# Optimization experiments

Hardware: AMD Instinct MI355X
Metric: run time of the kernel (lower is better)

The kernel has to match this reference:

```python
import jax, jax.numpy as jnp
import numpy as np

D_MODEL = 256
D_INNER = 512   # expand_factor * d_model
D_STATE = 64
DT_RANK = 4     # ceil(d_model / 64)
D_CONV = 4
B = 8
L = 144


def setup_inputs() -> dict:
    key = jax.random.key(0)
    ks = jax.random.split(key, 8)
    s = lambda k, shp, sc=0.02: jax.random.normal(k, shp, jnp.float32) * sc
    x = jax.random.normal(ks[0], (B, L, D_MODEL), jnp.float32)
    lastin = jnp.zeros((B, D_INNER, D_STATE), jnp.float32)  # accepted but unused by the scan
    W_in = s(ks[1], (2 * D_INNER, D_MODEL))              # in_proj (no bias)
    conv_w = s(ks[2], (D_INNER, 1, D_CONV), 0.1)          # depthwise conv kernel [O, I/groups, K]
    conv_b = jnp.zeros((D_INNER,), jnp.float32)
    W_x = s(ks[3], (DT_RANK + 2 * D_STATE, D_INNER))      # x_proj (no bias)
    W_dt = s(ks[4], (D_INNER, DT_RANK), 0.1)
    b_dt = jnp.full((D_INNER,), -4.0, jnp.float32)        # softplus -> small dt, like mamba init
    A_log = jnp.log(jnp.tile(jnp.arange(1, D_STATE + 1, dtype=jnp.float32), (D_INNER, 1)))
    Dp = jnp.ones((D_INNER,), jnp.float32)
    W_out = s(ks[5], (D_MODEL, D_INNER))                  # out_proj (no bias)
    return dict(x=x, lastin=lastin, W_in=W_in, conv_w=conv_w, conv_b=conv_b,
                W_x=W_x, W_dt=W_dt, b_dt=b_dt, A_log=A_log, Dp=Dp, W_out=W_out)


def _forward(x, lastin, W_in, conv_w, conv_b, W_x, W_dt, b_dt, A_log, Dp, W_out):
    # in_proj and split
    xz = jnp.einsum('bld,ed->ble', x, W_in)               # [B, L, 2*d_inner]
    ix, z = jnp.split(xz, 2, axis=-1)

    # depthwise causal-ish conv1d: torch padding=2 then slice [:L] == padding (2, 1)
    ix = jnp.swapaxes(ix, 1, 2)                            # [B, d_inner, L]
    ix = jax.lax.conv_general_dilated(
        ix, conv_w, window_strides=(1,), padding=[(2, 1)],
        feature_group_count=D_INNER, dimension_numbers=('NCH', 'OIH', 'NCH'))
    ix = ix + conv_b[None, :, None]
    ix = jnp.swapaxes(ix, 1, 2)                            # [B, L, d_inner]
    ix = jax.nn.silu(ix)

    # ssm parameterization
    A = -jnp.exp(A_log)                                    # [d_inner, d_state]
    dBC = jnp.einsum('bld,ed->ble', ix, W_x)               # [B, L, dt_rank + 2*d_state]
    dt_r = dBC[..., :DT_RANK]
    Bm = dBC[..., DT_RANK:DT_RANK + D_STATE]               # [B, L, d_state]
    Cm = dBC[..., DT_RANK + D_STATE:]                      # [B, L, d_state]
    delta = jax.nn.softplus(jnp.einsum('blr,dr->bld', dt_r, W_dt) + b_dt)  # [B, L, d_inner]

    # discretization
    deltaA = jnp.exp(delta[..., None] * A)                 # [B, L, d_inner, d_state]
    BX = (delta * ix)[..., None] * Bm[:, :, None, :]       # [B, L, d_inner, d_state]

    # sequential selective scan: h_t = deltaA_t * h_{t-1} + BX_t
    def step(h, inp):
        dA_t, bx_t = inp
        h = dA_t * h + bx_t
        return h, h

    h0 = jnp.zeros((x.shape[0], D_INNER, D_STATE), x.dtype)
    _, hs = jax.lax.scan(step, h0, (jnp.moveaxis(deltaA, 1, 0), jnp.moveaxis(BX, 1, 0)))
    # hs: [L, B, d_inner, d_state]

    y = jnp.einsum('lbdn,lbn->bld', hs, jnp.moveaxis(Cm, 1, 0))  # [B, L, d_inner]
    y = y + Dp * ix

    out = jnp.einsum('bld,ed->ble', y * jax.nn.silu(z), W_out)   # [B, L, d_model]
    return out


def reference(x, lastin, W_in, conv_w, conv_b, W_x, W_dt, b_dt, A_log, Dp, W_out):
    return _forward(x, lastin, W_in, conv_w, conv_b, W_x, W_dt, b_dt, A_log, Dp, W_out)
```

## Files before the change

kernel.cpp:

```cpp
#include <hip/hip_runtime.h>
#include <hip/hip_bf16.h>

#define B_SZ 8
#define L_SEQ 144
#define NTOK 1152
#define D_MODEL 256
#define D_INNER 512
#define D_STATE 64
#define DT_RANK 4

typedef __attribute__((ext_vector_type(8))) short bf16x8;
typedef __attribute__((ext_vector_type(4))) float f32x4;
typedef __attribute__((ext_vector_type(4))) short short4v;

__device__ __forceinline__ unsigned short bf16_rn(float f) {
    unsigned u = __float_as_uint(f);
    u += 0x7FFF + ((u >> 16) & 1);
    return (unsigned short)(u >> 16);
}
__device__ __forceinline__ float bf16_f(unsigned short h) {
    return __uint_as_float(((unsigned)h) << 16);
}
__device__ __forceinline__ unsigned packsplit(float f) {
    const unsigned short h = bf16_rn(f);
    const unsigned short l = bf16_rn(f - bf16_f(h));
    return (unsigned)h | ((unsigned)l << 16);
}

#define LP 40

template<bool APACK, bool GN>
__global__ __launch_bounds__(256) void gemm_mfma(const void* __restrict__ Aptr,
                                                 const float* __restrict__ Bptr,
                                                 float* __restrict__ C,
                                                 const int N, const int K,
                                                 const int lda, const int ldb,
                                                 const int ldc) {
    __shared__ short Ah[64 * LP], Al[64 * LP], Bh[64 * LP], Bl[64 * LP];
    const float* Af = (const float*)Aptr;
    const unsigned* Au = (const unsigned*)Aptr;
    const int tid = threadIdx.x;
    const int m0 = blockIdx.y * 64;
    const int n0 = blockIdx.x * 64;
    const int w = tid >> 6, l = tid & 63;
    const int lm = l & 15, lq = l >> 4;
    const int m0w = (w >> 1) * 32, n0w = (w & 1) * 32;
    f32x4 acc[2][2] = {};

    for (int k0 = 0; k0 < K; k0 += 32) {
        unsigned short ha[2][4], la[2][4], hb[2][4], lb[2][4];
#pragma unroll
        for (int p = 0; p < 2; ++p) {
            const int i = tid + 256 * p;
            const int r = i >> 3, c = (i & 7) * 4;
            if (APACK) {
                const uint4 v = *(const uint4*)(Au + (size_t)(m0 + r) * lda + k0 + c);
                ha[p][0] = v.x & 0xFFFF; la[p][0] = v.x >> 16;
                ha[p][1] = v.y & 0xFFFF; la[p][1] = v.y >> 16;
                ha[p][2] = v.z & 0xFFFF; la[p][2] = v.z >> 16;
                ha[p][3] = v.w & 0xFFFF; la[p][3] = v.w >> 16;
            } else {
                const float4 v = *(const float4*)(Af + (size_t)(m0 + r) * lda + k0 + c);
                ha[p][0] = bf16_rn(v.x); la[p][0] = bf16_rn(v.x - bf16_f(ha[p][0]));
                ha[p][1] = bf16_rn(v.y); la[p][1] = bf16_rn(v.y - bf16_f(ha[p][1]));
                ha[p][2] = bf16_rn(v.z); la[p][2] = bf16_rn(v.z - bf16_f(ha[p][2]));
                ha[p][3] = bf16_rn(v.w); la[p][3] = bf16_rn(v.w - bf16_f(ha[p][3]));
            }
            float4 bv = make_float4(0.f, 0.f, 0.f, 0.f);
            if (!GN || (n0 + r) < N)
                bv = *(const float4*)(Bptr + (size_t)(n0 + r) * ldb + k0 + c);
            hb[p][0] = bf16_rn(bv.x); lb[p][0] = bf16_rn(bv.x - bf16_f(hb[p][0]));
            hb[p][1] = bf16_rn(bv.y); lb[p][1] = bf16_rn(bv.y - bf16_f(hb[p][1]));
            hb[p][2] = bf16_rn(bv.z); lb[p][2] = bf16_rn(bv.z - bf16_f(hb[p][2]));
            hb[p][3] = bf16_rn(bv.w); lb[p][3] = bf16_rn(bv.w - bf16_f(hb[p][3]));
        }
        __syncthreads();
#pragma unroll
        for (int p = 0; p < 2; ++p) {
            const int i = tid + 256 * p;
            const int r = i >> 3, c = (i & 7) * 4;
            const int o = r * LP + c;
            short4v v;
            v = (short4v){(short)ha[p][0], (short)ha[p][1], (short)ha[p][2], (short)ha[p][3]};
            *(short4v*)&Ah[o] = v;
            v = (short4v){(short)la[p][0], (short)la[p][1], (short)la[p][2], (short)la[p][3]};
            *(short4v*)&Al[o] = v;
            v = (short4v){(short)hb[p][0], (short)hb[p][1], (short)hb[p][2], (short)hb[p][3]};
            *(short4v*)&Bh[o] = v;
            v = (short4v){(short)lb[p][0], (short)lb[p][1], (short)lb[p][2], (short)lb[p][3]};
            *(short4v*)&Bl[o] = v;
        }
        __syncthreads();
        bf16x8 fah[2], fal[2], fbh[2], fbl[2];
#pragma unroll
        for (int t = 0; t < 2; ++t) {
            const int ao = (m0w + t * 16 + lm) * LP + lq * 8;
            fah[t] = *(const bf16x8*)&Ah[ao];
            fal[t] = *(const bf16x8*)&Al[ao];
            const int bo = (n0w + t * 16 + lm) * LP + lq * 8;
            fbh[t] = *(const bf16x8*)&Bh[bo];
            fbl[t] = *(const bf16x8*)&Bl[bo];
        }
#pragma unroll
        for (int mt = 0; mt < 2; ++mt)
#pragma unroll
            for (int nt = 0; nt < 2; ++nt) {
                acc[mt][nt] = __builtin_amdgcn_mfma_f32_16x16x32_bf16(
                    fal[mt], fbh[nt], acc[mt][nt], 0, 0, 0);
                acc[mt][nt] = __builtin_amdgcn_mfma_f32_16x16x32_bf16(
                    fah[mt], fbl[nt], acc[mt][nt], 0, 0, 0);
                acc[mt][nt] = __builtin_amdgcn_mfma_f32_16x16x32_bf16(
                    fah[mt], fbh[nt], acc[mt][nt], 0, 0, 0);
            }
    }
#pragma unroll
    for (int mt = 0; mt < 2; ++mt) {
        const int gm = m0 + m0w + mt * 16 + lq * 4;
#pragma unroll
        for (int nt = 0; nt < 2; ++nt) {
            const int gn = n0 + n0w + nt * 16 + lm;
            if (!GN || gn < N) {
#pragma unroll
                for (int r = 0; r < 4; ++r)
                    C[(size_t)(gm + r) * ldc + gn] = acc[mt][nt][r];
            }
        }
    }
}

__global__ __launch_bounds__(256) void transpack_k(const float* __restrict__ in,
                                                   unsigned* __restrict__ out) {
    __shared__ unsigned T[64][65];
    const int t0 = blockIdx.x * 64, d0 = blockIdx.y * 64;
    const int a = threadIdx.x & 15, g = threadIdx.x >> 4;
#pragma unroll
    for (int p = 0; p < 4; ++p) {
        const int d = g + 16 * p;
        const float4 v = *(const float4*)(in + (size_t)(d0 + d) * NTOK + t0 + a * 4);
        T[d][a * 4 + 0] = packsplit(v.x);
        T[d][a * 4 + 1] = packsplit(v.y);
        T[d][a * 4 + 2] = packsplit(v.z);
        T[d][a * 4 + 3] = packsplit(v.w);
    }
    __syncthreads();
#pragma unroll
    for (int p = 0; p < 4; ++p) {
        const int tt = g + 16 * p;
        uint4 o;
        o.x = T[a * 4 + 0][tt];
        o.y = T[a * 4 + 1][tt];
        o.z = T[a * 4 + 2][tt];
        o.w = T[a * 4 + 3][tt];
        *(uint4*)(out + (size_t)(t0 + tt) * D_INNER + d0 + a * 4) = o;
    }
}

__global__ __launch_bounds__(128) void conv_k(const float* __restrict__ xzT,
                                              const float* __restrict__ cw,
                                              const float* __restrict__ cb,
                                              float* __restrict__ ixT) {
    const int tok = blockIdx.x * 128 + threadIdx.x;
    const int d = blockIdx.y;
    const int b = tok / L_SEQ;
    const int t = tok - b * L_SEQ;
    const float* row = xzT + (size_t)d * NTOK + tok;
    const float4 w = *(const float4*)(cw + d * 4);
    float s = cb[d];
    if (t >= 2) s = fmaf(w.x, row[-2], s);
    if (t >= 1) s = fmaf(w.y, row[-1], s);
    s = fmaf(w.z, row[0], s);
    if (t < L_SEQ - 1) s = fmaf(w.w, row[1], s);
    ixT[(size_t)d * NTOK + tok] = s * __builtin_amdgcn_rcpf(1.f + __expf(-s));
}

template<int CNT>
__device__ __forceinline__ void scan_chunk(const float* __restrict__ dBC,
                                           const float* __restrict__ xzT,
                                           const float* __restrict__ ixT,
                                           float* __restrict__ gT,
                                           float4* __restrict__ aux_w,
                                           float (*__restrict__ Pw)[65],
                                           const int d, const int base, const int t0,
                                           const float An2, const float4 wdt,
                                           const float bdt, const float dpv,
                                           const int lane, float& h) {
    if (lane < CNT) {
        const int tok = base + t0 + lane;
        const float4 dt4 = *(const float4*)(dBC + (size_t)tok * 132);
        float s = fmaf(dt4.x, wdt.x, bdt);
        s = fmaf(dt4.y, wdt.y, s);
        s = fmaf(dt4.z, wdt.z, s);
        s = fmaf(dt4.w, wdt.w, s);
        const float delta = fmaxf(s, 0.f) + __logf(1.f + __expf(-fabsf(s)));
        const float ixv = ixT[(size_t)d * NTOK + tok];
        const float zv  = xzT[(size_t)(D_INNER + d) * NTOK + tok];
        const float sz  = zv * __builtin_amdgcn_rcpf(1.f + __expf(-zv));
        aux_w[lane] = make_float4(delta, delta * ixv, dpv * ixv, sz);
    }
#pragma unroll 8
    for (int i = 0; i < CNT; ++i) {
        const size_t rb = (size_t)(base + t0 + i) * 132;
        const float Bv = dBC[rb + DT_RANK + lane];
        const float Cv = dBC[rb + DT_RANK + D_STATE + lane];
        const float4 a4 = aux_w[i];
        const float dA = __builtin_amdgcn_exp2f(a4.x * An2);
        h = fmaf(dA, h, a4.y * Bv);
        Pw[i][lane] = h * Cv;
    }
    const int tl = lane & 31, hf = lane >> 5;
    float s2 = 0.f;
    if (tl < CNT) {
#pragma unroll
        for (int j = 0; j < 32; ++j) s2 += Pw[tl][hf * 32 + j];
    }
    s2 += __shfl_xor(s2, 32, 64);
    if (hf == 0 && tl < CNT) {
        const float4 a4 = aux_w[tl];
        gT[(size_t)d * NTOK + base + t0 + tl] = (s2 + a4.z) * a4.w;
    }
}

__global__ __launch_bounds__(256) void scan_k(const float* __restrict__ dBC,
                                              const float* __restrict__ xzT,
                                              const float* __restrict__ ixT,
                                              const float* __restrict__ W_dt,
                                              const float* __restrict__ b_dt,
                                              const float* __restrict__ A_log,
                                              const float* __restrict__ Dp,
                                              float* __restrict__ gT) {
    __shared__ float4 aux_s[4][32];
    __shared__ float P[4][32][65];
    const int w = threadIdx.x >> 6, lane = threadIdx.x & 63;
    const int b = blockIdx.x >> 7, dg = blockIdx.x & 127;
    const int d = (dg << 2) | w;
    const int base = b * L_SEQ;
    const float An2 = -__expf(A_log[(d << 6) + lane]) * 1.44269504088896f;
    const float4 wdt = *(const float4*)(W_dt + (d << 2));
    const float bdt = b_dt[d], dpv = Dp[d];
    float h = 0.f;
    scan_chunk<32>(dBC, xzT, ixT, gT, aux_s[w], P[w], d, base, 0,  An2, wdt, bdt, dpv, lane, h);
    scan_chunk<32>(dBC, xzT, ixT, gT, aux_s[w], P[w], d, base, 32, An2, wdt, bdt, dpv, lane, h);
    scan_chunk<32>(dBC, xzT, ixT, gT, aux_s[w], P[w], d, base, 64, An2, wdt, bdt, dpv, lane, h);
    scan_chunk<32>(dBC, xzT, ixT, gT, aux_s[w], P[w], d, base, 96, An2, wdt, bdt, dpv, lane, h);
    scan_chunk<16>(dBC, xzT, ixT, gT, aux_s[w], P[w], d, base, 128, An2, wdt, bdt, dpv, lane, h);
}

extern "C" void kernel_launch(void* const* d_in, const int* in_sizes, int n_in,
                              void* d_out, int out_size, void* d_ws, size_t ws_size,
                              hipStream_t stream) {
    const float* x      = (const float*)d_in[0];
    const float* W_in   = (const float*)d_in[2];
    const float* conv_w = (const float*)d_in[3];
    const float* conv_b = (const float*)d_in[4];
    const float* W_x    = (const float*)d_in[5];
    const float* W_dt   = (const float*)d_in[6];
    const float* b_dt   = (const float*)d_in[7];
    const float* A_log  = (const float*)d_in[8];
    const float* Dp     = (const float*)d_in[9];
    const float* W_out  = (const float*)d_in[10];
    float* out = (float*)d_out;

    float* ws  = (float*)d_ws;
    float* xzT = ws;
    float* ixT = xzT + 1179648;
    float* dBC = ixT + 589824;
    float* gT  = dBC + 152064;
    unsigned* ixM = (unsigned*)(gT + 589824);
    unsigned* gM  = ixM + 589824;

    gemm_mfma<false, false><<<dim3(18, 16), 256, 0, stream>>>(
        W_in, x, xzT, NTOK, D_MODEL, D_MODEL, D_MODEL, NTOK);
    conv_k<<<dim3(9, D_INNER), 128, 0, stream>>>(xzT, conv_w, conv_b, ixT);
    transpack_k<<<dim3(18, 8), 256, 0, stream>>>(ixT, ixM);
    gemm_mfma<true, true><<<dim3(3, 18), 256, 0, stream>>>(
        ixM, W_x, dBC, 132, D_INNER, D_INNER, D_INNER, 132);
    scan_k<<<dim3(B_SZ * 128), 256, 0, stream>>>(dBC, xzT, ixT, W_dt, b_dt, A_log, Dp, gT);
    transpack_k<<<dim3(18, 8), 256, 0, stream>>>(gT, gM);
    gemm_mfma<true, false><<<dim3(4, 18), 256, 0, stream>>>(
        gM, W_out, out, D_MODEL, D_INNER, D_INNER, D_INNER, D_MODEL);
}
```

Baseline: 144.1 us.

## Fuse pipeline into cooperative persistent kernel with grid syncs

Replaces the seven separate launches with one cooperative persistent kernel whose phases (in_proj GEMM, conv, x_proj GEMM, scan, out_proj GEMM) are separated by grid-wide barriers. The conv and scan phases now write the packed bf16 hi/lo transposed operands directly, so the two transpose-pack kernels go away. The scan is re-chunked into 16-token pieces to cut shared memory so two blocks fit per CU, capped at 512 blocks. This removes launch overhead and intermediate round trips, but adds grid.sync costs, uncoalesced strided packed stores, and a fixed grid that may underuse the GPU in the GEMM phases.

```diff
diff --git a/kernel.cpp b/kernel.cpp
--- a/kernel.cpp
+++ b/kernel.cpp
@@ -1,5 +1,7 @@
 #include <hip/hip_runtime.h>
-#include <hip/hip_bf16.h>
+#include <hip/hip_cooperative_groups.h>
+
+namespace cg = cooperative_groups;
 
 #define B_SZ 8
 #define L_SEQ 144
@@ -8,6 +10,8 @@
 #define D_INNER 512
 #define D_STATE 64
 #define DT_RANK 4
+#define LP 40
+#define NTHR 256
 
 typedef __attribute__((ext_vector_type(8))) short bf16x8;
 typedef __attribute__((ext_vector_type(4))) float f32x4;
@@ -27,21 +31,18 @@
     return (unsigned)h | ((unsigned)l << 16);
 }
 
-#define LP 40
-
 template<bool APACK, bool GN>
-__global__ __launch_bounds__(256) void gemm_mfma(const void* __restrict__ Aptr,
-                                                 const float* __restrict__ Bptr,
-                                                 float* __restrict__ C,
-                                                 const int N, const int K,
-                                                 const int lda, const int ldb,
-                                                 const int ldc) {
-    __shared__ short Ah[64 * LP], Al[64 * LP], Bh[64 * LP], Bl[64 * LP];
+__device__ __forceinline__ void gemm_tile(const void* __restrict__ Aptr,
+                                          const float* __restrict__ Bptr,
+                                          float* __restrict__ C,
+                                          const int N, const int K,
+                                          const int lda, const int ldb, const int ldc,
+                                          const int m0, const int n0,
+                                          short* __restrict__ Ah, short* __restrict__ Al,
+                                          short* __restrict__ Bh, short* __restrict__ Bl) {
     const float* Af = (const float*)Aptr;
     const unsigned* Au = (const unsigned*)Aptr;
     const int tid = threadIdx.x;
-    const int m0 = blockIdx.y * 64;
-    const int n0 = blockIdx.x * 64;
     const int w = tid >> 6, l = tid & 63;
     const int lm = l & 15, lq = l >> 4;
     const int m0w = (w >> 1) * 32, n0w = (w & 1) * 32;
@@ -128,121 +129,175 @@
     }
 }
 
-__global__ __launch_bounds__(256) void transpack_k(const float* __restrict__ in,
-                                                   unsigned* __restrict__ out) {
-    __shared__ unsigned T[64][65];
-    const int t0 = blockIdx.x * 64, d0 = blockIdx.y * 64;
-    const int a = threadIdx.x & 15, g = threadIdx.x >> 4;
-#pragma unroll
-    for (int p = 0; p < 4; ++p) {
-        const int d = g + 16 * p;
-        const float4 v = *(const float4*)(in + (size_t)(d0 + d) * NTOK + t0 + a * 4);
-        T[d][a * 4 + 0] = packsplit(v.x);
-        T[d][a * 4 + 1] = packsplit(v.y);
-        T[d][a * 4 + 2] = packsplit(v.z);
-        T[d][a * 4 + 3] = packsplit(v.w);
-    }
-    __syncthreads();
-#pragma unroll
-    for (int p = 0; p < 4; ++p) {
-        const int tt = g + 16 * p;
-        uint4 o;
-        o.x = T[a * 4 + 0][tt];
-        o.y = T[a * 4 + 1][tt];
-        o.z = T[a * 4 + 2][tt];
-        o.w = T[a * 4 + 3][tt];
-        *(uint4*)(out + (size_t)(t0 + tt) * D_INNER + d0 + a * 4) = o;
-    }
-}
-
-__global__ __launch_bounds__(128) void conv_k(const float* __restrict__ xzT,
-                                              const float* __restrict__ cw,
-                                              const float* __restrict__ cb,
-                                              float* __restrict__ ixT) {
-    const int tok = blockIdx.x * 128 + threadIdx.x;
-    const int d = blockIdx.y;
-    const int b = tok / L_SEQ;
-    const int t = tok - b * L_SEQ;
-    const float* row = xzT + (size_t)d * NTOK + tok;
-    const float4 w = *(const float4*)(cw + d * 4);
-    float s = cb[d];
-    if (t >= 2) s = fmaf(w.x, row[-2], s);
-    if (t >= 1) s = fmaf(w.y, row[-1], s);
-    s = fmaf(w.z, row[0], s);
-    if (t < L_SEQ - 1) s = fmaf(w.w, row[1], s);
-    ixT[(size_t)d * NTOK + tok] = s * __builtin_amdgcn_rcpf(1.f + __expf(-s));
-}
-
-template<int CNT>
-__device__ __forceinline__ void scan_chunk(const float* __restrict__ dBC,
-                                           const float* __restrict__ xzT,
-                                           const float* __restrict__ ixT,
-                                           float* __restrict__ gT,
-                                           float4* __restrict__ aux_w,
-                                           float (*__restrict__ Pw)[65],
-                                           const int d, const int base, const int t0,
-                                           const float An2, const float4 wdt,
-                                           const float bdt, const float dpv,
-                                           const int lane, float& h) {
-    if (lane < CNT) {
-        const int tok = base + t0 + lane;
-        const float4 dt4 = *(const float4*)(dBC + (size_t)tok * 132);
-        float s = fmaf(dt4.x, wdt.x, bdt);
-        s = fmaf(dt4.y, wdt.y, s);
-        s = fmaf(dt4.z, wdt.z, s);
-        s = fmaf(dt4.w, wdt.w, s);
-        const float delta = fmaxf(s, 0.f) + __logf(1.f + __expf(-fabsf(s)));
-        const float ixv = ixT[(size_t)d * NTOK + tok];
-        const float zv  = xzT[(size_t)(D_INNER + d) * NTOK + tok];
-        const float sz  = zv * __builtin_amdgcn_rcpf(1.f + __expf(-zv));
-        aux_w[lane] = make_float4(delta, delta * ixv, dpv * ixv, sz);
-    }
+__device__ __forceinline__ void phase_gemm1(int blk, int gsz,
+        const float* W_in, const float* x, float* xzT,
+        short* Ah, short* Al, short* Bh, short* Bl) {
+    for (int t = blk; t < 288; t += gsz) {
+        const int bx = t % 18, by = t / 18;
+        gemm_tile<false, false>(W_in, x, xzT, NTOK, D_MODEL, D_MODEL, D_MODEL, NTOK,
+                                by * 64, bx * 64, Ah, Al, Bh, Bl);
+    }
+}
+
+__device__ __forceinline__ void phase_conv(int blk, int gsz,
+        const float* xzT, const float* conv_w, const float* conv_b,
+        float* ixT, unsigned* ixM) {
+    for (int idx = blk * NTHR + threadIdx.x; idx < D_INNER * NTOK; idx += gsz * NTHR) {
+        const int d = idx / NTOK;
+        const int tok = idx - d * NTOK;
+        const int b = tok / L_SEQ;
+        const int t = tok - b * L_SEQ;
+        const float* row = xzT + (size_t)d * NTOK + tok;
+        const float4 cw4 = *(const float4*)(conv_w + d * 4);
+        float s = conv_b[d];
+        if (t >= 2) s = fmaf(cw4.x, row[-2], s);
+        if (t >= 1) s = fmaf(cw4.y, row[-1], s);
+        s = fmaf(cw4.z, row[0], s);
+        if (t < L_SEQ - 1) s = fmaf(cw4.w, row[1], s);
+        const float r = s * __builtin_amdgcn_rcpf(1.f + __expf(-s));
+        ixT[idx] = r;
+        ixM[(size_t)tok * D_INNER + d] = packsplit(r);
+    }
+}
+
+__device__ __forceinline__ void phase_gemm3(int blk, int gsz,
+        const unsigned* ixM, const float* W_x, float* dBC,
+        short* Ah, short* Al, short* Bh, short* Bl) {
+    for (int t = blk; t < 54; t += gsz) {
+        const int bx = t % 3, by = t / 3;
+        gemm_tile<true, true>(ixM, W_x, dBC, 132, D_INNER, D_INNER, D_INNER, 132,
+                              by * 64, bx * 64, Ah, Al, Bh, Bl);
+    }
+}
+
+__device__ __forceinline__ void phase_scan(int blk, int gsz,
+        const float* dBC, const float* xzT, const float* ixT,
+        const float* W_dt, const float* b_dt, const float* A_log,
+        const float* Dp, unsigned* gM, char* smem) {
+    float4* aux_s = (float4*)smem;
+    float* Pb = (float*)(smem + 1024);
+    const int w = threadIdx.x >> 6, lane = threadIdx.x & 63;
+    float4* aux_w = aux_s + w * 16;
+    float (*Pw)[65] = (float(*)[65])(Pb + w * 16 * 65);
+    for (int u = blk; u < 1024; u += gsz) {
+        const int b = u >> 7, dg = u & 127;
+        const int d = (dg << 2) | w;
+        const int base = b * L_SEQ;
+        const float An2 = -__expf(A_log[(d << 6) + lane]) * 1.44269504088896f;
+        const float4 wdt = *(const float4*)(W_dt + (d << 2));
+        const float bdt = b_dt[d], dpv = Dp[d];
+        float h = 0.f;
+#pragma unroll 1
+        for (int c = 0; c < 9; ++c) {
+            const int t0 = c * 16;
+            if (lane < 16) {
+                const int tok = base + t0 + lane;
+                const float4 dt4 = *(const float4*)(dBC + (size_t)tok * 132);
+                float s = fmaf(dt4.x, wdt.x, bdt);
+                s = fmaf(dt4.y, wdt.y, s);
+                s = fmaf(dt4.z, wdt.z, s);
+                s = fmaf(dt4.w, wdt.w, s);
+                const float delta = fmaxf(s, 0.f) + __logf(1.f + __expf(-fabsf(s)));
+                const float ixv = ixT[(size_t)d * NTOK + tok];
+                const float zv  = xzT[(size_t)(D_INNER + d) * NTOK + tok];
+                const float sz  = zv * __builtin_amdgcn_rcpf(1.f + __expf(-zv));
+                aux_w[lane] = make_float4(delta, delta * ixv, dpv * ixv, sz);
+            }
 #pragma unroll 8
-    for (int i = 0; i < CNT; ++i) {
-        const size_t rb = (size_t)(base + t0 + i) * 132;
-        const float Bv = dBC[rb + DT_RANK + lane];
-        const float Cv = dBC[rb + DT_RANK + D_STATE + lane];
-        const float4 a4 = aux_w[i];
-        const float dA = __builtin_amdgcn_exp2f(a4.x * An2);
-        h = fmaf(dA, h, a4.y * Bv);
-        Pw[i][lane] = h * Cv;
-    }
-    const int tl = lane & 31, hf = lane >> 5;
-    float s2 = 0.f;
-    if (tl < CNT) {
-#pragma unroll
-        for (int j = 0; j < 32; ++j) s2 += Pw[tl][hf * 32 + j];
-    }
-    s2 += __shfl_xor(s2, 32, 64);
-    if (hf == 0 && tl < CNT) {
-        const float4 a4 = aux_w[tl];
-        gT[(size_t)d * NTOK + base + t0 + tl] = (s2 + a4.z) * a4.w;
-    }
-}
-
-__global__ __launch_bounds__(256) void scan_k(const float* __restrict__ dBC,
-                                              const float* __restrict__ xzT,
-                                              const float* __restrict__ ixT,
-                                              const float* __restrict__ W_dt,
-                                              const float* __restrict__ b_dt,
-                                              const float* __restrict__ A_log,
-                                              const float* __restrict__ Dp,
-                                              float* __restrict__ gT) {
-    __shared__ float4 aux_s[4][32];
-    __shared__ float P[4][32][65];
-    const int w = threadIdx.x >> 6, lane = threadIdx.x & 63;
-    const int b = blockIdx.x >> 7, dg = blockIdx.x & 127;
-    const int d = (dg << 2) | w;
-    const int base = b * L_SEQ;
-    const float An2 = -__expf(A_log[(d << 6) + lane]) * 1.44269504088896f;
-    const float4 wdt = *(const float4*)(W_dt + (d << 2));
-    const float bdt = b_dt[d], dpv = Dp[d];
-    float h = 0.f;
-    scan_chunk<32>(dBC, xzT, ixT, gT, aux_s[w], P[w], d, base, 0,  An2, wdt, bdt, dpv, lane, h);
-    scan_chunk<32>(dBC, xzT, ixT, gT, aux_s[w], P[w], d, base, 32, An2, wdt, bdt, dpv, lane, h);
-    scan_chunk<32>(dBC, xzT, ixT, gT, aux_s[w], P[w], d, base, 64, An2, wdt, bdt, dpv, lane, h);
-    scan_chunk<32>(dBC, xzT, ixT, gT, aux_s[w], P[w], d, base, 96, An2, wdt, bdt, dpv, lane, h);
-    scan_chunk<16>(dBC, xzT, ixT, gT, aux_s[w], P[w], d, base, 128, An2, wdt, bdt, dpv, lane, h);
+            for (int i = 0; i < 16; ++i) {
+                const size_t rb = (size_t)(base + t0 + i) * 132;
+                const float Bv = dBC[rb + DT_RANK + lane];
+                const float Cv = dBC[rb + DT_RANK + D_STATE + lane];
+                const float4 a4 = aux_w[i];
+                const float dA = __builtin_amdgcn_exp2f(a4.x * An2);
+                h = fmaf(dA, h, a4.y * Bv);
+                Pw[i][lane] = h * Cv;
+            }
+            const int tl = lane & 31, hf = lane >> 5;
+            float s2 = 0.f;
+            if (tl < 16) {
+#pragma unroll
+                for (int j = 0; j < 32; ++j) s2 += Pw[tl][hf * 32 + j];
+            }
+            s2 += __shfl_xor(s2, 32, 64);
+            if (hf == 0 && tl < 16) {
+                const float4 a4 = aux_w[tl];
+                gM[(size_t)(base + t0 + tl) * D_INNER + d] =
+                    packsplit((s2 + a4.z) * a4.w);
+            }
+        }
+    }
+}
+
+__device__ __forceinline__ void phase_gemm7(int blk, int gsz,
+        const unsigned* gM, const float* W_out, float* out,
+        short* Ah, short* Al, short* Bh, short* Bl) {
+    for (int t = blk; t < 72; t += gsz) {
+        const int bx = t % 4, by = t / 4;
+        gemm_tile<true, false>(gM, W_out, out, D_MODEL, D_INNER, D_INNER, D_INNER,
+                               D_MODEL, by * 64, bx * 64, Ah, Al, Bh, Bl);
+    }
+}
+
+__global__ __launch_bounds__(NTHR, 2) void mega_k(
+        const float* __restrict__ x, const float* __restrict__ W_in,
+        const float* __restrict__ conv_w, const float* __restrict__ conv_b,
+        const float* __restrict__ W_x, const float* __restrict__ W_dt,
+        const float* __restrict__ b_dt, const float* __restrict__ A_log,
+        const float* __restrict__ Dp, const float* __restrict__ W_out,
+        float* __restrict__ out,
+        float* __restrict__ xzT, float* __restrict__ ixT,
+        unsigned* __restrict__ ixM, float* __restrict__ dBC,
+        unsigned* __restrict__ gM) {
+    __shared__ __align__(16) char smem[4 * 64 * LP * 2];
+    short* Ah = (short*)smem;
+    short* Al = Ah + 64 * LP;
+    short* Bh = Al + 64 * LP;
+    short* Bl = Bh + 64 * LP;
+    cg::grid_group grid = cg::this_grid();
+    const int blk = blockIdx.x, gsz = gridDim.x;
+
+    phase_gemm1(blk, gsz, W_in, x, xzT, Ah, Al, Bh, Bl);
+    grid.sync();
+    phase_conv(blk, gsz, xzT, conv_w, conv_b, ixT, ixM);
+    grid.sync();
+    phase_gemm3(blk, gsz, ixM, W_x, dBC, Ah, Al, Bh, Bl);
+    grid.sync();
+    phase_scan(blk, gsz, dBC, xzT, ixT, W_dt, b_dt, A_log, Dp, gM, smem);
+    grid.sync();
+    phase_gemm7(blk, gsz, gM, W_out, out, Ah, Al, Bh, Bl);
+}
+
+#define SMEM_DECL __shared__ __align__(16) char smem[4 * 64 * LP * 2]; \
+    short* Ah = (short*)smem; short* Al = Ah + 64 * LP; \
+    short* Bh = Al + 64 * LP; short* Bl = Bh + 64 * LP;
+
+__global__ __launch_bounds__(NTHR, 2) void k1(const float* W_in, const float* x,
+                                              float* xzT) {
+    SMEM_DECL;
+    phase_gemm1(blockIdx.x, gridDim.x, W_in, x, xzT, Ah, Al, Bh, Bl);
+}
+__global__ __launch_bounds__(NTHR, 2) void k2(const float* xzT, const float* cw,
+                                              const float* cb, float* ixT,
+                                              unsigned* ixM) {
+    phase_conv(blockIdx.x, gridDim.x, xzT, cw, cb, ixT, ixM);
+}
+__global__ __launch_bounds__(NTHR, 2) void k3(const unsigned* ixM, const float* W_x,
+                                              float* dBC) {
+    SMEM_DECL;
+    phase_gemm3(blockIdx.x, gridDim.x, ixM, W_x, dBC, Ah, Al, Bh, Bl);
+}
+__global__ __launch_bounds__(NTHR, 2) void k4(const float* dBC, const float* xzT,
+                                              const float* ixT, const float* W_dt,
+                                              const float* b_dt, const float* A_log,
+                                              const float* Dp, unsigned* gM) {
+    __shared__ __align__(16) char smem[4 * 64 * LP * 2];
+    phase_scan(blockIdx.x, gridDim.x, dBC, xzT, ixT, W_dt, b_dt, A_log, Dp, gM, smem);
+}
+__global__ __launch_bounds__(NTHR, 2) void k5(const unsigned* gM, const float* W_out,
+                                              float* out) {
+    SMEM_DECL;
+    phase_gemm7(blockIdx.x, gridDim.x, gM, W_out, out, Ah, Al, Bh, Bl);
 }
 
 extern "C" void kernel_launch(void* const* d_in, const int* in_sizes, int n_in,
@@ -264,18 +319,33 @@
     float* xzT = ws;
     float* ixT = xzT + 1179648;
     float* dBC = ixT + 589824;
-    float* gT  = dBC + 152064;
-    unsigned* ixM = (unsigned*)(gT + 589824);
+    unsigned* ixM = (unsigned*)(dBC + 152064);
     unsigned* gM  = ixM + 589824;
 
-    gemm_mfma<false, false><<<dim3(18, 16), 256, 0, stream>>>(
-        W_in, x, xzT, NTOK, D_MODEL, D_MODEL, D_MODEL, NTOK);
-    conv_k<<<dim3(9, D_INNER), 128, 0, stream>>>(xzT, conv_w, conv_b, ixT);
-    transpack_k<<<dim3(18, 8), 256, 0, stream>>>(ixT, ixM);
-    gemm_mfma<true, true><<<dim3(3, 18), 256, 0, stream>>>(
-        ixM, W_x, dBC, 132, D_INNER, D_INNER, D_INNER, 132);
-    scan_k<<<dim3(B_SZ * 128), 256, 0, stream>>>(dBC, xzT, ixT, W_dt, b_dt, A_log, Dp, gT);
-    transpack_k<<<dim3(18, 8), 256, 0, stream>>>(gT, gM);
-    gemm_mfma<true, false><<<dim3(4, 18), 256, 0, stream>>>(
-        gM, W_out, out, D_MODEL, D_INNER, D_INNER, D_INNER, D_MODEL);
-}
+    int dev = 0;
+    (void)hipGetDevice(&dev);
+    int coop = 0;
+    (void)hipDeviceGetAttribute(&coop, hipDeviceAttributeCooperativeLaunch, dev);
+    int maxBlk = 0;
+    if (hipOccupancyMaxActiveBlocksPerMultiprocessor(&maxBlk, mega_k, NTHR, 0)
+        != hipSuccess) maxBlk = 0;
+
+    if (coop && maxBlk >= 1) {
+        int grid = maxBlk * 256;
+        if (grid > 512) grid = 512;
+        void* params[] = {
+            (void*)&x, (void*)&W_in, (void*)&conv_w, (void*)&conv_b, (void*)&W_x,
+            (void*)&W_dt, (void*)&b_dt, (void*)&A_log, (void*)&Dp, (void*)&W_out,
+            (void*)&out, (void*)&xzT, (void*)&ixT, (void*)&ixM, (void*)&dBC,
+            (void*)&gM
+        };
+        (void)hipLaunchCooperativeKernel((void*)mega_k, dim3(grid), dim3(NTHR),
+                                         params, 0, stream);
+    } else {
+        k1<<<dim3(288), NTHR, 0, stream>>>(W_in, x, xzT);
+        k2<<<dim3(512), NTHR, 0, stream>>>(xzT, conv_w, conv_b, ixT, ixM);
+        k3<<<dim3(54),  NTHR, 0, stream>>>(ixM, W_x, dBC);
+        k4<<<dim3(512), NTHR, 0, stream>>>(dBC, xzT, ixT, W_dt, b_dt, A_log, Dp, gM);
+        k5<<<dim3(72),  NTHR, 0, stream>>>(gM, W_out, out);
+    }
+}
```

After: 394.0 us. +173.4%, slower.

## Fuse conv+SiLU into transpose-pack and write scan output pre-packed

Applied to the files above, without the earlier changes.

The depthwise conv and SiLU are folded into the transpose/bf16-split packing kernel, so the separate fp32 ixT buffer and its kernel are gone. The scan now reads ix from the packed token-major buffer and writes its gated output straight in packed split-bf16 form, which removes the second transpack launch. The pipeline drops from seven kernels to five and writes less intermediate data, but the scan's ix reads and g writes become strided (token-major with stride D_INNER), which may coalesce worse. The ix value now comes from the hi+lo bf16 split rather than exact fp32.

```diff
diff --git a/kernel.cpp b/kernel.cpp
--- a/kernel.cpp
+++ b/kernel.cpp
@@ -1,5 +1,4 @@
 #include <hip/hip_runtime.h>
-#include <hip/hip_bf16.h>
 
 #define B_SZ 8
 #define L_SEQ 144
@@ -8,6 +7,8 @@
 #define D_INNER 512
 #define D_STATE 64
 #define DT_RANK 4
+#define LP 40
+#define NTHR 256
 
 typedef __attribute__((ext_vector_type(8))) short bf16x8;
 typedef __attribute__((ext_vector_type(4))) float f32x4;
@@ -26,22 +27,22 @@
     const unsigned short l = bf16_rn(f - bf16_f(h));
     return (unsigned)h | ((unsigned)l << 16);
 }
-
-#define LP 40
+__device__ __forceinline__ float unpacksum(unsigned p) {
+    return bf16_f((unsigned short)(p & 0xFFFF)) + bf16_f((unsigned short)(p >> 16));
+}
 
 template<bool APACK, bool GN>
-__global__ __launch_bounds__(256) void gemm_mfma(const void* __restrict__ Aptr,
-                                                 const float* __restrict__ Bptr,
-                                                 float* __restrict__ C,
-                                                 const int N, const int K,
-                                                 const int lda, const int ldb,
-                                                 const int ldc) {
-    __shared__ short Ah[64 * LP], Al[64 * LP], Bh[64 * LP], Bl[64 * LP];
+__device__ __forceinline__ void gemm_tile(const void* __restrict__ Aptr,
+                                          const float* __restrict__ Bptr,
+                                          float* __restrict__ C,
+                                          const int N, const int K,
+                                          const int lda, const int ldb, const int ldc,
+                                          const int m0, const int n0,
+                                          short* __restrict__ Ah, short* __restrict__ Al,
+                                          short* __restrict__ Bh, short* __restrict__ Bl) {
     const float* Af = (const float*)Aptr;
     const unsigned* Au = (const unsigned*)Aptr;
     const int tid = threadIdx.x;
-    const int m0 = blockIdx.y * 64;
-    const int n0 = blockIdx.x * 64;
     const int w = tid >> 6, l = tid & 63;
     const int lm = l & 15, lq = l >> 4;
     const int m0w = (w >> 1) * 32, n0w = (w & 1) * 32;
@@ -128,19 +129,52 @@
     }
 }
 
-__global__ __launch_bounds__(256) void transpack_k(const float* __restrict__ in,
-                                                   unsigned* __restrict__ out) {
+#define SMEM_DECL __shared__ __align__(16) char smem[4 * 64 * LP * 2]; \
+    short* Ah = (short*)smem; short* Al = Ah + 64 * LP; \
+    short* Bh = Al + 64 * LP; short* Bl = Bh + 64 * LP;
+
+__global__ __launch_bounds__(NTHR, 2) void k1(const float* __restrict__ W_in,
+                                              const float* __restrict__ x,
+                                              float* __restrict__ xzT) {
+    SMEM_DECL;
+    const int t = blockIdx.x;
+    const int bx = t % 18, by = t / 18;
+    gemm_tile<false, false>(W_in, x, xzT, NTOK, D_MODEL, D_MODEL, D_MODEL, NTOK,
+                            by * 64, bx * 64, Ah, Al, Bh, Bl);
+}
+
+__global__ __launch_bounds__(NTHR) void k2(const float* __restrict__ xzT,
+                                           const float* __restrict__ cw,
+                                           const float* __restrict__ cb,
+                                           unsigned* __restrict__ ixM) {
     __shared__ unsigned T[64][65];
     const int t0 = blockIdx.x * 64, d0 = blockIdx.y * 64;
     const int a = threadIdx.x & 15, g = threadIdx.x >> 4;
 #pragma unroll
     for (int p = 0; p < 4; ++p) {
-        const int d = g + 16 * p;
-        const float4 v = *(const float4*)(in + (size_t)(d0 + d) * NTOK + t0 + a * 4);
-        T[d][a * 4 + 0] = packsplit(v.x);
-        T[d][a * 4 + 1] = packsplit(v.y);
-        T[d][a * 4 + 2] = packsplit(v.z);
-        T[d][a * 4 + 3] = packsplit(v.w);
+        const int d = d0 + g + 16 * p;
+        const int tokbase = t0 + a * 4;
+        const float* row = xzT + (size_t)d * NTOK + tokbase;
+        const float4 w = *(const float4*)(cw + d * 4);
+        const float bias = cb[d];
+        float xv[7];
+        xv[0] = (tokbase >= 2) ? row[-2] : 0.f;
+        xv[1] = (tokbase >= 1) ? row[-1] : 0.f;
+        const float4 v = *(const float4*)row;
+        xv[2] = v.x; xv[3] = v.y; xv[4] = v.z; xv[5] = v.w;
+        xv[6] = (tokbase + 4 < NTOK) ? row[4] : 0.f;
+#pragma unroll
+        for (int j = 0; j < 4; ++j) {
+            const int tok = tokbase + j;
+            const int t = tok - (tok / L_SEQ) * L_SEQ;
+            float s = bias;
+            if (t >= 2) s = fmaf(w.x, xv[j], s);
+            if (t >= 1) s = fmaf(w.y, xv[j + 1], s);
+            s = fmaf(w.z, xv[j + 2], s);
+            if (t < L_SEQ - 1) s = fmaf(w.w, xv[j + 3], s);
+            const float r = s * __builtin_amdgcn_rcpf(1.f + __expf(-s));
+            T[g + 16 * p][a * 4 + j] = packsplit(r);
+        }
     }
     __syncthreads();
 #pragma unroll
@@ -151,33 +185,25 @@
         o.y = T[a * 4 + 1][tt];
         o.z = T[a * 4 + 2][tt];
         o.w = T[a * 4 + 3][tt];
-        *(uint4*)(out + (size_t)(t0 + tt) * D_INNER + d0 + a * 4) = o;
-    }
-}
-
-__global__ __launch_bounds__(128) void conv_k(const float* __restrict__ xzT,
-                                              const float* __restrict__ cw,
-                                              const float* __restrict__ cb,
-                                              float* __restrict__ ixT) {
-    const int tok = blockIdx.x * 128 + threadIdx.x;
-    const int d = blockIdx.y;
-    const int b = tok / L_SEQ;
-    const int t = tok - b * L_SEQ;
-    const float* row = xzT + (size_t)d * NTOK + tok;
-    const float4 w = *(const float4*)(cw + d * 4);
-    float s = cb[d];
-    if (t >= 2) s = fmaf(w.x, row[-2], s);
-    if (t >= 1) s = fmaf(w.y, row[-1], s);
-    s = fmaf(w.z, row[0], s);
-    if (t < L_SEQ - 1) s = fmaf(w.w, row[1], s);
-    ixT[(size_t)d * NTOK + tok] = s * __builtin_amdgcn_rcpf(1.f + __expf(-s));
+        *(uint4*)(ixM + (size_t)(t0 + tt) * D_INNER + d0 + a * 4) = o;
+    }
+}
+
+__global__ __launch_bounds__(NTHR, 2) void k3(const unsigned* __restrict__ ixM,
+                                              const float* __restrict__ W_x,
+                                              float* __restrict__ dBC) {
+    SMEM_DECL;
+    const int t = blockIdx.x;
+    const int bx = t % 3, by = t / 3;
+    gemm_tile<true, true>(ixM, W_x, dBC, 132, D_INNER, D_INNER, D_INNER, 132,
+                          by * 64, bx * 64, Ah, Al, Bh, Bl);
 }
 
 template<int CNT>
 __device__ __forceinline__ void scan_chunk(const float* __restrict__ dBC,
                                            const float* __restrict__ xzT,
-                                           const float* __restrict__ ixT,
-                                           float* __restrict__ gT,
+                                           const unsigned* __restrict__ ixM,
+                                           unsigned* __restrict__ gM,
                                            float4* __restrict__ aux_w,
                                            float (*__restrict__ Pw)[65],
                                            const int d, const int base, const int t0,
@@ -192,7 +218,7 @@
         s = fmaf(dt4.z, wdt.z, s);
         s = fmaf(dt4.w, wdt.w, s);
         const float delta = fmaxf(s, 0.f) + __logf(1.f + __expf(-fabsf(s)));
-        const float ixv = ixT[(size_t)d * NTOK + tok];
+        const float ixv = unpacksum(ixM[(size_t)tok * D_INNER + d]);
         const float zv  = xzT[(size_t)(D_INNER + d) * NTOK + tok];
         const float sz  = zv * __builtin_amdgcn_rcpf(1.f + __expf(-zv));
         aux_w[lane] = make_float4(delta, delta * ixv, dpv * ixv, sz);
@@ -216,18 +242,18 @@
     s2 += __shfl_xor(s2, 32, 64);
     if (hf == 0 && tl < CNT) {
         const float4 a4 = aux_w[tl];
-        gT[(size_t)d * NTOK + base + t0 + tl] = (s2 + a4.z) * a4.w;
-    }
-}
-
-__global__ __launch_bounds__(256) void scan_k(const float* __restrict__ dBC,
-                                              const float* __restrict__ xzT,
-                                              const float* __restrict__ ixT,
-                                              const float* __restrict__ W_dt,
-                                              const float* __restrict__ b_dt,
-                                              const float* __restrict__ A_log,
-                                              const float* __restrict__ Dp,
-                                              float* __restrict__ gT) {
+        gM[(size_t)(base + t0 + tl) * D_INNER + d] = packsplit((s2 + a4.z) * a4.w);
+    }
+}
+
+__global__ __launch_bounds__(NTHR) void k4(const float* __restrict__ dBC,
+                                           const float* __restrict__ xzT,
+                                           const unsigned* __restrict__ ixM,
+                                           const float* __restrict__ W_dt,
+                                           const float* __restrict__ b_dt,
+                                           const float* __restrict__ A_log,
+                                           const float* __restrict__ Dp,
+                                           unsigned* __restrict__ gM) {
     __shared__ float4 aux_s[4][32];
     __shared__ float P[4][32][65];
     const int w = threadIdx.x >> 6, lane = threadIdx.x & 63;
@@ -237,12 +263,24 @@
     const float An2 = -__expf(A_log[(d << 6) + lane]) * 1.44269504088896f;
     const float4 wdt = *(const float4*)(W_dt + (d << 2));
     const float bdt = b_dt[d], dpv = Dp[d];
+    float4* aux_w = aux_s[w];
+    float (*Pw)[65] = P[w];
     float h = 0.f;
-    scan_chunk<32>(dBC, xzT, ixT, gT, aux_s[w], P[w], d, base, 0,  An2, wdt, bdt, dpv, lane, h);
-    scan_chunk<32>(dBC, xzT, ixT, gT, aux_s[w], P[w], d, base, 32, An2, wdt, bdt, dpv, lane, h);
-    scan_chunk<32>(dBC, xzT, ixT, gT, aux_s[w], P[w], d, base, 64, An2, wdt, bdt, dpv, lane, h);
-    scan_chunk<32>(dBC, xzT, ixT, gT, aux_s[w], P[w], d, base, 96, An2, wdt, bdt, dpv, lane, h);
-    scan_chunk<16>(dBC, xzT, ixT, gT, aux_s[w], P[w], d, base, 128, An2, wdt, bdt, dpv, lane, h);
+    scan_chunk<32>(dBC, xzT, ixM, gM, aux_w, Pw, d, base, 0,   An2, wdt, bdt, dpv, lane, h);
+    scan_chunk<32>(dBC, xzT, ixM, gM, aux_w, Pw, d, base, 32,  An2, wdt, bdt, dpv, lane, h);
+    scan_chunk<32>(dBC, xzT, ixM, gM, aux_w, Pw, d, base, 64,  An2, wdt, bdt, dpv, lane, h);
+    scan_chunk<32>(dBC, xzT, ixM, gM, aux_w, Pw, d, base, 96,  An2, wdt, bdt, dpv, lane, h);
+    scan_chunk<16>(dBC, xzT, ixM, gM, aux_w, Pw, d, base, 128, An2, wdt, bdt, dpv, lane, h);
+}
+
+__global__ __launch_bounds__(NTHR, 2) void k5(const unsigned* __restrict__ gM,
+                                              const float* __restrict__ W_out,
+                                              float* __restrict__ out) {
+    SMEM_DECL;
+    const int t = blockIdx.x;
+    const int bx = t % 4, by = t / 4;
+    gemm_tile<true, false>(gM, W_out, out, D_MODEL, D_INNER, D_INNER, D_INNER,
+                           D_MODEL, by * 64, bx * 64, Ah, Al, Bh, Bl);
 }
 
 extern "C" void kernel_launch(void* const* d_in, const int* in_sizes, int n_in,
@@ -262,20 +300,13 @@
 
     float* ws  = (float*)d_ws;
     float* xzT = ws;
-    float* ixT = xzT + 1179648;
-    float* dBC = ixT + 589824;
-    float* gT  = dBC + 152064;
-    unsigned* ixM = (unsigned*)(gT + 589824);
+    float* dBC = xzT + 1179648;
+    unsigned* ixM = (unsigned*)(dBC + 152064);
     unsigned* gM  = ixM + 589824;
 
-    gemm_mfma<false, false><<<dim3(18, 16), 256, 0, stream>>>(
-        W_in, x, xzT, NTOK, D_MODEL, D_MODEL, D_MODEL, NTOK);
-    conv_k<<<dim3(9, D_INNER), 128, 0, stream>>>(xzT, conv_w, conv_b, ixT);
-    transpack_k<<<dim3(18, 8), 256, 0, stream>>>(ixT, ixM);
-    gemm_mfma<true, true><<<dim3(3, 18), 256, 0, stream>>>(
-        ixM, W_x, dBC, 132, D_INNER, D_INNER, D_INNER, 132);
-    scan_k<<<dim3(B_SZ * 128), 256, 0, stream>>>(dBC, xzT, ixT, W_dt, b_dt, A_log, Dp, gT);
-    transpack_k<<<dim3(18, 8), 256, 0, stream>>>(gT, gM);
-    gemm_mfma<true, false><<<dim3(4, 18), 256, 0, stream>>>(
-        gM, W_out, out, D_MODEL, D_INNER, D_INNER, D_INNER, D_MODEL);
-}
+    k1<<<dim3(288), NTHR, 0, stream>>>(W_in, x, xzT);
+    k2<<<dim3(18, 8), NTHR, 0, stream>>>(xzT, conv_w, conv_b, ixM);
+    k3<<<dim3(54), NTHR, 0, stream>>>(ixM, W_x, dBC);
+    k4<<<dim3(1024), NTHR, 0, stream>>>(dBC, xzT, ixM, W_dt, b_dt, A_log, Dp, gM);
+    k5<<<dim3(72), NTHR, 0, stream>>>(gM, W_out, out);
+}
```

Measured after the change: 141.3 us. Within noise of the previous version (-1.9%).
